# Kernel tuning notes

Hardware: AMD Instinct MI355X
Metric: run time of the kernel (lower is better)

Reference implementation:

```python
import jax, jax.numpy as jnp
import numpy as np

C = 512
CQ = C // 8
BN_EPS = 1e-5


def setup_inputs() -> dict:
    key = jax.random.key(0)
    ks = jax.random.split(key, 12)
    s = 0.02
    return {
        "x": jax.random.normal(ks[0], (4, C, 64, 64), dtype=jnp.float32),
        "qw": jax.random.normal(ks[1], (CQ, C), dtype=jnp.float32) * s,
        "qb": jnp.zeros((CQ,), dtype=jnp.float32),
        "kw": jax.random.normal(ks[2], (CQ, C), dtype=jnp.float32) * s,
        "kb": jnp.zeros((CQ,), dtype=jnp.float32),
        "vw": jax.random.normal(ks[3], (C, C), dtype=jnp.float32) * s,
        "vb": jnp.zeros((C,), dtype=jnp.float32),
        "gamma": jnp.zeros((1,), dtype=jnp.float32),
        "beta": jnp.zeros((1,), dtype=jnp.float32),
        "fw": jax.random.normal(ks[4], (C, 2 * C), dtype=jnp.float32) * s,
        "fb": jnp.zeros((C,), dtype=jnp.float32),
        "bn_w": jnp.ones((C,), dtype=jnp.float32),
        "bn_b": jnp.zeros((C,), dtype=jnp.float32),
    }


def reference(x, qw, qb, kw, kb, vw, vb, gamma, beta, fw, fb, bn_w, bn_b):
    b, c, h, w = x.shape
    n = h * w
    xf = x.reshape(b, c, n)  # [b, c, n]

    # ----- position attention -----
    q = jnp.einsum('oc,bcn->bon', qw, xf) + qb[None, :, None]  # [b, cq, n]
    k = jnp.einsum('oc,bcn->bon', kw, xf) + kb[None, :, None]
    v = jnp.einsum('oc,bcn->bon', vw, xf) + vb[None, :, None]  # [b, c, n]
    # scores[i, j] = q_i . k_j, softmax over j
    scores = jnp.einsum('bci,bcj->bij', q, k)  # [b, n, n]
    att = jax.nn.softmax(scores, axis=-1)
    pos = jnp.einsum('bcj,bij->bci', v, att)  # [b, c, n]
    pos_out = (gamma[0] * pos + xf).reshape(b, c, h, w)

    # ----- channel attention -----
    energy = jnp.einsum('bin,bjn->bij', xf, xf)  # [b, c, c]
    catt = jax.nn.softmax(energy, axis=-1)
    chan = jnp.einsum('bij,bjn->bin', catt, xf)
    chan_out = (beta[0] * chan + xf).reshape(b, c, h, w)

    # ----- fusion: 1x1 conv + BN (batch stats, training mode) + ReLU -----
    cat = jnp.concatenate([pos_out, chan_out], axis=1)  # [b, 2c, h, w]
    y = jnp.einsum('oc,bchw->bohw', fw, cat) + fb[None, :, None, None]
    mean = jnp.mean(y, axis=(0, 2, 3), keepdims=True)
    var = jnp.var(y, axis=(0, 2, 3), keepdims=True)
    yn = (y - mean) * jax.lax.rsqrt(var + BN_EPS)
    out = jax.nn.relu(yn * bn_w[None, :, None, None] + bn_b[None, :, None, None])
    return out
```

## Files before the change

kernel.cpp:

```cpp
#include <hip/hip_runtime.h>
#include <stdint.h>

typedef unsigned short u16;
typedef __attribute__((ext_vector_type(8))) short bf16x8;
typedef __attribute__((ext_vector_type(4))) float f32x4;

#define DEVI static __device__ __forceinline__

DEVI u16 f2bf(float f){
  union { float f; uint32_t u; } c; c.f = f;
  uint32_t u = c.u;
  u += 0x7FFFu + ((u >> 16) & 1u);
  return (u16)(u >> 16);
}
DEVI float b2f(u16 h){
  union { uint32_t u; float f; } c; c.u = ((uint32_t)h) << 16;
  return c.f;
}

DEVI void gload16(const u16* g, u16* l){
  __builtin_amdgcn_global_load_lds(
      (const __attribute__((address_space(1))) unsigned int*)g,
      (__attribute__((address_space(3))) unsigned int*)l, 16, 0, 0);
}

DEVI bf16x8 ldsrd(const void* base, int byte){
  return *reinterpret_cast<const bf16x8*>((const char*)base + byte);
}

template<int BM,int BN,int FM,int FN,int BIAS,int EPI,int SWZ,int KSPLIT=1>
__global__ __launch_bounds__(256) void gemm_bt(
    const u16* __restrict__ A, long long strideA, int lda,
    const u16* __restrict__ B, long long strideB, int ldb,
    void* __restrict__ C, long long strideC, int ldc,
    const float* __restrict__ bias, int K,
    const float* __restrict__ cscale, const u16* __restrict__ xadd,
    long long strideX, int ldx, float* __restrict__ red)
{
  constexpr int BK  = 32;
  constexpr int WTM = FM*16, WTN = FN*16;
  static_assert(BM == 2*WTM && BN == 2*WTN, "2x2 wave layout");
  __shared__ u16 As[BM*BK];
  __shared__ u16 Bs[BN*BK];

  int bx = blockIdx.x, by = blockIdx.y, bz = blockIdx.z;
  if(SWZ){
    const int gx = gridDim.x, gy = gridDim.y;
    const int nwg = gx * gy * gridDim.z;
    const int orig = bx + gx * (by + gy * bz);
    const int q = nwg >> 3, r = nwg & 7;
    const int xcd = orig & 7, i = orig >> 3;
    const int wg = (xcd < r ? xcd*(q+1) : r*(q+1) + (xcd-r)*q) + i;
    bx = wg % gx;
    const int t = wg / gx;
    by = t % gy;
    bz = t / gy;
  }

  const int zz = bz;
  const int z  = (KSPLIT > 1) ? zz / KSPLIT : zz;
  const int ks = (KSPLIT > 1) ? zz % KSPLIT : 0;
  const u16* Ab = A + (long long)z * strideA + (long long)ks * K;
  const u16* Bb = B + (long long)z * strideB + (long long)ks * K;

  const int tid  = threadIdx.x;
  const int lane = tid & 63, wid = tid >> 6;
  const int wr = wid >> 1, wc = wid & 1;
  const long long bm0 = (long long)by * BM;
  const long long bn0 = (long long)bx * BN;

  const int srow  = lane >> 2;
  const int scol  = (((lane & 3) ^ ((lane >> 3) & 3))) * 8;
  const int wrow  = wid * 16 + srow;
  constexpr int TA = BM/64, TB = BN/64;

  const int fr  = lane & 15;
  const int sl8 = ((lane >> 4) ^ ((lane >> 1) & 3)) * 8;

  f32x4 acc[FM][FN] = {};

  for(int k0 = 0; k0 < K; k0 += BK){
    __syncthreads();
    #pragma unroll
    for(int t=0;t<TA;t++)
      gload16(&Ab[(bm0 + t*64 + wrow)*lda + k0 + scol],
              &As[(t*64 + wid*16)*BK]);
    #pragma unroll
    for(int t=0;t<TB;t++)
      gload16(&Bb[(bn0 + t*64 + wrow)*ldb + k0 + scol],
              &Bs[(t*64 + wid*16)*BK]);
    __syncthreads();

    bf16x8 af[FM], bg[FN];
    #pragma unroll
    for(int m=0;m<FM;m++)
      af[m] = *reinterpret_cast<const bf16x8*>(&As[(wr*WTM + m*16 + fr)*BK + sl8]);
    #pragma unroll
    for(int n=0;n<FN;n++)
      bg[n] = *reinterpret_cast<const bf16x8*>(&Bs[(wc*WTN + n*16 + fr)*BK + sl8]);
    #pragma unroll
    for(int m=0;m<FM;m++)
      #pragma unroll
      for(int n=0;n<FN;n++)
        acc[m][n] = __builtin_amdgcn_mfma_f32_16x16x32_bf16(af[m], bg[n], acc[m][n], 0, 0, 0);
  }

  const int lr = (lane >> 4) * 4, lc = lane & 15;

  if(EPI == 7){
    u16* Cp = (u16*)C + (long long)zz*strideC;
    #pragma unroll
    for(int m=0;m<FM;m++){
      #pragma unroll
      for(int r=0;r<4;r++){
        long long row = bm0 + wr*WTM + m*16 + lr + r;
        float bv = bias[(int)row];
        float s = 0.f, ss = 0.f;
        #pragma unroll
        for(int n=0;n<FN;n++){
          long long col = bn0 + wc*WTN + n*16 + lc;
          float v = acc[m][n][r] + bv;
          Cp[row*(long long)ldc + col] = f2bf(v);
          s += v; ss += v*v;
        }
        #pragma unroll
        for(int o=1;o<16;o<<=1){ s += __shfl_xor(s, o); ss += __shfl_xor(ss, o); }
        if(lc == 0){
          int slot = (z*(int)gridDim.x + bx)*2 + wc;
          red[(int)row*512 + slot*2]     = s;
          red[(int)row*512 + slot*2 + 1] = ss;
        }
      }
    }
    return;
  }

  const float g = (EPI == 3) ? cscale[0] : 0.f;
  #pragma unroll
  for(int m=0;m<FM;m++){
    #pragma unroll
    for(int n=0;n<FN;n++){
      #pragma unroll
      for(int r=0;r<4;r++){
        long long row = bm0 + wr*WTM + m*16 + lr + r;
        long long col = bn0 + wc*WTN + n*16 + lc;
        float v = acc[m][n][r];
        if(BIAS == 1) v += bias[(int)row];
        if(BIAS == 2) v += bias[(int)col];
        long long idx = row * (long long)ldc + col;
        if(EPI == 0){
          ((float*)C + (long long)zz*strideC)[idx] = v;
        } else if(EPI == 1){
          ((float*)C + (long long)zz*strideC)[idx] += v;
        } else if(EPI == 2){
          ((u16*)C + (long long)zz*strideC)[idx] = f2bf(v);
        } else {
          float xv = b2f(xadd[(long long)z*strideX + row*(long long)ldx + col]);
          ((u16*)C + (long long)zz*strideC)[idx] = f2bf(g * v + xv);
        }
      }
    }
  }
}

__global__ __launch_bounds__(512, 4) void flash_pos(
    const u16* __restrict__ qkT,
    const u16* __restrict__ vB,
    const u16* __restrict__ xfT,
    u16* __restrict__ pcT,
    const float* __restrict__ gamma)
{
  __shared__ u16 Ks[2][64*64];
  __shared__ u16 Vs[256*64];
  __shared__ u16 Ps[64*64];
  __shared__ float RS[2][4][32];

  int flat = blockIdx.x + 64*(blockIdx.y + 2*blockIdx.z);
  flat = (flat & 7)*64 + (flat >> 3);
  const int bx = flat & 63;
  const int ch = (flat >> 6) & 1;
  const int z  = flat >> 7;

  const int q0 = bx*64, c0 = ch*256;
  const int tid = threadIdx.x, lane = tid & 63, wid = tid >> 6;
  const int wr = wid >> 2, wc = wid & 3;
  const int fr = lane & 15, fq = lane >> 4;

  const u16* qkb = qkT + (long long)z*4096*128;
  const u16* vbb = vB  + (long long)z*512*4096;

  const int srow  = lane >> 3;
  const int sslot = (lane & 7) ^ srow;

  bf16x8 qa[2][2];
  #pragma unroll
  for(int m=0;m<2;m++)
    #pragma unroll
    for(int kk=0;kk<2;kk++)
      qa[m][kk] = *reinterpret_cast<const bf16x8*>(
          &qkb[(long long)(q0 + wr*32 + m*16 + fr)*128 + kk*32 + fq*8]);

  const u16* kp  = qkb + (long long)(wid*8 + srow)*128 + 64 + sslot*8;
  const u16* vp0 = vbb + (long long)(c0 + wid*8 + srow)*4096 + sslot*8;

  const int xm   = (fr & 7) << 4;
  const int koff = (wc*16 + fr)*128 + ((fq*16) ^ xm);
  const int pab  = (wr*32 + fr)*128 + ((fq*16) ^ xm);
  const int vfb  = (wc*64 + fr)*128 + ((fq*16) ^ xm);
  const int kdst = wid * 1024;
  const int key2 = (wc*16 + fr)*2;
  int pwo[4];
  #pragma unroll
  for(int r=0;r<4;r++){
    int qr = fq*4 + r;
    pwo[r] = qr*128 + (key2 ^ ((qr & 7) << 4));
  }

  gload16(kp, (u16*)((char*)Ks + kdst));
  kp += 64*128;
  gload16(vp0,            &Vs[(  0 + wid*8)*64]);
  gload16(vp0 +  64*4096, &Vs[( 64 + wid*8)*64]);
  gload16(vp0 + 128*4096, &Vs[(128 + wid*8)*64]);
  gload16(vp0 + 192*4096, &Vs[(192 + wid*8)*64]);
  vp0 += 64;
  __syncthreads();

  f32x4 acc[2][4] = {};
  float rsacc[2][4] = {};

  for(int t=0;t<64;t++){
    const int kbase = (t & 1) ? 8192 : 0;
    bf16x8 kb0 = ldsrd(Ks, kbase + koff);
    bf16x8 kb1 = ldsrd(Ks, kbase + (koff ^ 64));
    f32x4 s[2] = {};
    #pragma unroll
    for(int m=0;m<2;m++){
      s[m] = __builtin_amdgcn_mfma_f32_16x16x32_bf16(qa[m][0], kb0, s[m], 0, 0, 0);
      s[m] = __builtin_amdgcn_mfma_f32_16x16x32_bf16(qa[m][1], kb1, s[m], 0, 0, 0);
    }

    #pragma unroll
    for(int m=0;m<2;m++){
      #pragma unroll
      for(int r=0;r<4;r++){
        float e = __expf(s[m][r]);
        rsacc[m][r] += e;
        *(u16*)((char*)Ps + (pwo[r] + wr*4096 + m*2048)) = f2bf(e);
      }
    }
    __syncthreads();

    if(t+1 < 64){
      gload16(kp, (u16*)((char*)Ks + (kbase ^ 8192) + kdst));
      kp += 64*128;
    }

    bf16x8 pa00 = ldsrd(Ps, pab);
    bf16x8 pa01 = ldsrd(Ps, pab ^ 64);
    bf16x8 pa10 = ldsrd(Ps, (pab + 2048));
    bf16x8 pa11 = ldsrd(Ps, (pab + 2048) ^ 64);
    __builtin_amdgcn_s_setprio(1);
    #pragma unroll
    for(int n=0;n<4;n++){
      bf16x8 v0 = ldsrd(Vs, vfb + n*2048);
      bf16x8 v1 = ldsrd(Vs, (vfb + n*2048) ^ 64);
      acc[0][n] = __builtin_amdgcn_mfma_f32_16x16x32_bf16(pa00, v0, acc[0][n], 0, 0, 0);
      acc[0][n] = __builtin_amdgcn_mfma_f32_16x16x32_bf16(pa01, v1, acc[0][n], 0, 0, 0);
      acc[1][n] = __builtin_amdgcn_mfma_f32_16x16x32_bf16(pa10, v0, acc[1][n], 0, 0, 0);
      acc[1][n] = __builtin_amdgcn_mfma_f32_16x16x32_bf16(pa11, v1, acc[1][n], 0, 0, 0);
    }
    __builtin_amdgcn_s_setprio(0);
    __syncthreads();

    if(t+1 < 64){
      gload16(vp0,            &Vs[(  0 + wid*8)*64]);
      gload16(vp0 +  64*4096, &Vs[( 64 + wid*8)*64]);
      gload16(vp0 + 128*4096, &Vs[(128 + wid*8)*64]);
      gload16(vp0 + 192*4096, &Vs[(192 + wid*8)*64]);
      vp0 += 64;
    }
  }

  #pragma unroll
  for(int m=0;m<2;m++)
    #pragma unroll
    for(int r=0;r<4;r++){
      float v = rsacc[m][r];
      #pragma unroll
      for(int o=1;o<16;o<<=1) v += __shfl_xor(v, o);
      rsacc[m][r] = v;
    }
  if(fr == 0){
    #pragma unroll
    for(int m=0;m<2;m++)
      #pragma unroll
      for(int r=0;r<4;r++)
        RS[wr][wc][m*16 + fq*4 + r] = rsacc[m][r];
  }
  __syncthreads();

  const float g = gamma[0];
  #pragma unroll
  for(int m=0;m<2;m++){
    float inv[4];
    #pragma unroll
    for(int r=0;r<4;r++){
      int rloc = m*16 + fq*4 + r;
      inv[r] = g / (RS[wr][0][rloc] + RS[wr][1][rloc] +
                    RS[wr][2][rloc] + RS[wr][3][rloc]);
    }
    #pragma unroll
    for(int n=0;n<4;n++){
      #pragma unroll
      for(int r=0;r<4;r++){
        int qrow = q0 + wr*32 + m*16 + fq*4 + r;
        int c    = c0 + wc*64 + n*16 + fr;
        float xv = b2f(xfT[((long long)z*4096 + qrow)*512 + c]);
        pcT[((long long)z*4096 + qrow)*1024 + c] = f2bf(acc[m][n][r]*inv[r] + xv);
      }
    }
  }
}

__global__ __launch_bounds__(256) void softmax_sum8b(const u16* __restrict__ part,
                                                     u16* __restrict__ catt)
{
  const int row = blockIdx.x;
  const int b = row >> 9, i = row & 511;
  const int t = threadIdx.x;
  const int lane = t & 63, wid = t >> 6;
  float v0 = 0.f, v1 = 0.f;
  #pragma unroll
  for(int sl=0;sl<8;sl++){
    uint32_t pr = *reinterpret_cast<const uint32_t*>(
        &part[(((long long)(b*8 + sl)*512 + i)*512) + 2*t]);
    v0 += b2f((u16)pr);
    v1 += b2f((u16)(pr >> 16));
  }
  float m = fmaxf(v0, v1);
  #pragma unroll
  for(int o=32;o;o>>=1) m = fmaxf(m, __shfl_xor(m, o));
  __shared__ float sred[4];
  if(lane == 0) sred[wid] = m;
  __syncthreads();
  m = fmaxf(fmaxf(sred[0], sred[1]), fmaxf(sred[2], sred[3]));
  float e0 = __expf(v0 - m), e1 = __expf(v1 - m);
  float s = e0 + e1;
  #pragma unroll
  for(int o=32;o;o>>=1) s += __shfl_xor(s, o);
  __syncthreads();
  if(lane == 0) sred[wid] = s;
  __syncthreads();
  s = sred[0] + sred[1] + sred[2] + sred[3];
  float inv = 1.0f / s;
  uint32_t pk = (uint32_t)f2bf(e0 * inv) | ((uint32_t)f2bf(e1 * inv) << 16);
  *reinterpret_cast<uint32_t*>(&catt[(long long)row * 512 + 2*t]) = pk;
}

__global__ __launch_bounds__(256) void prep_weights(
    const float* __restrict__ qw, const float* __restrict__ kw,
    const float* __restrict__ vw, const float* __restrict__ fw,
    const float* __restrict__ qb, const float* __restrict__ kb,
    u16* __restrict__ qkwb, u16* __restrict__ vwb, u16* __restrict__ fwb,
    float* __restrict__ qkb)
{
  long long i = (long long)blockIdx.x*256 + threadIdx.x;
  const float* src; u16* dst; long long o;
  if(i < 8192){        src = qw; dst = qkwb;          o = i; }
  else if(i < 16384){  src = kw; dst = qkwb + 32768;  o = i - 8192; }
  else if(i < 81920){  src = vw; dst = vwb;           o = i - 16384; }
  else if(i < 212992){ src = fw; dst = fwb;           o = i - 81920; }
  else if(i < 213024){
    int t = (int)(i - 212992) * 4;
    #pragma unroll
    for(int j=0;j<4;j++) qkb[t+j] = (t+j < 64) ? qb[t+j] : kb[t+j-64];
    return;
  } else return;
  float4 v = reinterpret_cast<const float4*>(src)[o];
  ushort4 w;
  w.x = f2bf(v.x); w.y = f2bf(v.y); w.z = f2bf(v.z); w.w = f2bf(v.w);
  reinterpret_cast<ushort4*>(dst)[o] = w;
}

__global__ __launch_bounds__(256) void transpose_cast(
    const float* __restrict__ x, u16* __restrict__ xfb, u16* __restrict__ xfT)
{
  __shared__ float tile[32][33];
  const int b  = blockIdx.z;
  const int n0 = blockIdx.x * 32, c0 = blockIdx.y * 32;
  const int tx = threadIdx.x, ty = threadIdx.y;
  const float* xp = x + (long long)b * 512 * 4096;
  #pragma unroll
  for(int i=0;i<4;i++){
    int c = c0 + ty + i*8;
    float v = xp[(long long)c*4096 + n0 + tx];
    tile[ty + i*8][tx] = v;
    xfb[((long long)b*512 + c)*4096 + n0 + tx] = f2bf(v);
  }
  __syncthreads();
  #pragma unroll
  for(int i=0;i<4;i++){
    int n = n0 + ty + i*8;
    xfT[((long long)b*4096 + n)*512 + c0 + tx] = f2bf(tile[tx][ty + i*8]);
  }
}

__global__ __launch_bounds__(256) void bn_finalize(const float* __restrict__ red,
                                                   float* __restrict__ stat)
{
  int ch = blockIdx.x*256 + threadIdx.x;
  if(ch >= 512) return;
  float s = 0.f, ss = 0.f;
  for(int j=0;j<256;j++){
    s  += red[ch*512 + j*2];
    ss += red[ch*512 + j*2 + 1];
  }
  float mean = s * (1.f/16384.f);
  float var  = ss * (1.f/16384.f) - mean*mean;
  stat[ch*2]   = mean;
  stat[ch*2+1] = rsqrtf(var + 1e-5f);
}

__global__ __launch_bounds__(256) void bn_apply_b(const u16* __restrict__ y,
    const float* __restrict__ stat, const float* __restrict__ w,
    const float* __restrict__ bb, float* __restrict__ out)
{
  long long i = (long long)blockIdx.x*256 + threadIdx.x;
  bf16x8 v = *reinterpret_cast<const bf16x8*>(&y[i*8]);
  int o = (int)(((i*8) >> 12) & 511);
  float sc = w[o] * stat[o*2+1];
  float sh = bb[o] - stat[o*2] * sc;
  float4 lo, hi;
  lo.x = fmaxf(b2f((u16)v[0])*sc + sh, 0.f);
  lo.y = fmaxf(b2f((u16)v[1])*sc + sh, 0.f);
  lo.z = fmaxf(b2f((u16)v[2])*sc + sh, 0.f);
  lo.w = fmaxf(b2f((u16)v[3])*sc + sh, 0.f);
  hi.x = fmaxf(b2f((u16)v[4])*sc + sh, 0.f);
  hi.y = fmaxf(b2f((u16)v[5])*sc + sh, 0.f);
  hi.z = fmaxf(b2f((u16)v[6])*sc + sh, 0.f);
  hi.w = fmaxf(b2f((u16)v[7])*sc + sh, 0.f);
  *reinterpret_cast<float4*>(&out[i*8])     = lo;
  *reinterpret_cast<float4*>(&out[i*8 + 4]) = hi;
}

extern "C" void kernel_launch(void* const* d_in, const int* in_sizes, int n_in,
                              void* d_out, int out_size, void* d_ws, size_t ws_size,
                              hipStream_t stream)
{
  const float* x     = (const float*)d_in[0];
  const float* qw    = (const float*)d_in[1];
  const float* qb    = (const float*)d_in[2];
  const float* kw    = (const float*)d_in[3];
  const float* kb    = (const float*)d_in[4];
  const float* vw    = (const float*)d_in[5];
  const float* vb    = (const float*)d_in[6];
  const float* gamma = (const float*)d_in[7];
  const float* beta  = (const float*)d_in[8];
  const float* fw    = (const float*)d_in[9];
  const float* fb    = (const float*)d_in[10];
  const float* bnw   = (const float*)d_in[11];
  const float* bnb   = (const float*)d_in[12];
  float* out = (float*)d_out;
  (void)in_sizes; (void)n_in; (void)out_size; (void)ws_size;

  char* base = (char*)d_ws;
  size_t off = 0;
  auto alloc = [&](size_t bytes)->char* {
    char* p = base + off;
    off += (bytes + 255) & ~(size_t)255;
    return p;
  };
  const long long NB = 4, Cc = 512, Nn = 4096;

  u16*   xfT  = (u16*)alloc((size_t)NB*Nn*Cc*2);
  u16*   fwb  = (u16*)alloc((size_t)Cc*2*Cc*2);
  char*  region = (char*)(base + off);
  u16*   xfb  = (u16*)alloc((size_t)NB*Cc*Nn*2);
  u16*   qkwb = (u16*)alloc((size_t)128*Cc*2);
  float* qkb  = (float*)alloc(128*4);
  u16*   vwb  = (u16*)alloc((size_t)Cc*Cc*2);
  u16*   qkT  = (u16*)alloc((size_t)NB*Nn*128*2);
  u16*   vB   = (u16*)alloc((size_t)NB*Cc*Nn*2);
  u16*   pcT  = (u16*)alloc((size_t)NB*Nn*1024*2);
  u16*   epart= (u16*)alloc((size_t)32*Cc*Cc*2);
  u16*   catt = (u16*)alloc((size_t)NB*Cc*Cc*2);
  float* stat = (float*)alloc((size_t)Cc*2*4);
  float* red  = (float*)alloc((size_t)Cc*256*2*4);
  u16*   ybf16= (u16*)region;

  prep_weights<<<dim3(833), dim3(256), 0, stream>>>(qw, kw, vw, fw, qb, kb,
                                                    qkwb, vwb, fwb, qkb);
  transpose_cast<<<dim3(128,16,4), dim3(32,8), 0, stream>>>(x, xfb, xfT);

  gemm_bt<64,128,2,4,2,2,1><<<dim3(1,64,4), dim3(256), 0, stream>>>(
      xfT, Nn*Cc, 512, qkwb, 0, 512, qkT, Nn*128, 128, qkb, 512,
      nullptr, nullptr, 0, 0, nullptr);
  gemm_bt<128,128,4,4,1,2,1><<<dim3(32,4,4), dim3(256), 0, stream>>>(
      vwb, 0, 512, xfT, Nn*Cc, 512, vB, Cc*Nn, 4096, vb, 512,
      nullptr, nullptr, 0, 0, nullptr);

  gemm_bt<128,128,4,4,0,2,1,8><<<dim3(4,4,32), dim3(256), 0, stream>>>(
      xfb, Cc*Nn, 4096, xfb, Cc*Nn, 4096, epart, Cc*Cc, 512, nullptr, 512,
      nullptr, nullptr, 0, 0, nullptr);
  softmax_sum8b<<<dim3(2048), dim3(256), 0, stream>>>(epart, catt);
  gemm_bt<128,128,4,4,0,3,1><<<dim3(4,32,4), dim3(256), 0, stream>>>(
      xfT, Nn*Cc, 512, catt, Cc*Cc, 512, pcT + 512, Nn*1024, 1024, nullptr, 512,
      beta, xfT, Nn*Cc, 512, nullptr);

  flash_pos<<<dim3(64,2,4), dim3(512), 0, stream>>>(qkT, vB, xfT, pcT, gamma);

  gemm_bt<128,128,4,4,1,7,1><<<dim3(32,4,4), dim3(256), 0, stream>>>(
      fwb, 0, 1024, pcT, Nn*1024, 1024, ybf16, Cc*Nn, 4096, fb, 1024,
      nullptr, nullptr, 0, 0, red);

  bn_finalize<<<dim3(2), dim3(256), 0, stream>>>(red, stat);
  bn_apply_b<<<dim3(4096), dim3(256), 0, stream>>>(ybf16, stat, bnw, bnb, out);
}
```

Baseline: 252.7 us.

## Compute fusion GEMM transposed, reduce BN stats per column, transpose in apply

The final 1x1-conv GEMM now has the spatial dimension as rows and output channels as columns, writing a transposed bf16 intermediate with column bias. BN partial sums are reduced down rows per column using fewer shuffles. bn_finalize is parallelized to one block per channel with a wave-shuffle reduction, and bn_apply becomes an LDS-tiled transpose back to NCHW. This trades a cheaper GEMM epilogue and finalize for a less efficient strided, transposing apply kernel.

```diff
diff --git a/kernel.cpp b/kernel.cpp
--- a/kernel.cpp
+++ b/kernel.cpp
@@ -107,29 +107,29 @@
 
   const int lr = (lane >> 4) * 4, lc = lane & 15;
 
-  if(EPI == 7){
+  if(EPI == 9){
     u16* Cp = (u16*)C + (long long)zz*strideC;
     #pragma unroll
-    for(int m=0;m<FM;m++){
-      #pragma unroll
-      for(int r=0;r<4;r++){
-        long long row = bm0 + wr*WTM + m*16 + lr + r;
-        float bv = bias[(int)row];
-        float s = 0.f, ss = 0.f;
+    for(int n=0;n<FN;n++){
+      long long col = bn0 + wc*WTN + n*16 + lc;
+      float bv = bias[(int)col];
+      float s = 0.f, ss = 0.f;
+      #pragma unroll
+      for(int m=0;m<FM;m++){
         #pragma unroll
-        for(int n=0;n<FN;n++){
-          long long col = bn0 + wc*WTN + n*16 + lc;
+        for(int r=0;r<4;r++){
+          long long row = bm0 + wr*WTM + m*16 + lr + r;
           float v = acc[m][n][r] + bv;
           Cp[row*(long long)ldc + col] = f2bf(v);
           s += v; ss += v*v;
         }
-        #pragma unroll
-        for(int o=1;o<16;o<<=1){ s += __shfl_xor(s, o); ss += __shfl_xor(ss, o); }
-        if(lc == 0){
-          int slot = (z*(int)gridDim.x + bx)*2 + wc;
-          red[(int)row*512 + slot*2]     = s;
-          red[(int)row*512 + slot*2 + 1] = ss;
-        }
+      }
+      s += __shfl_xor(s,16); ss += __shfl_xor(ss,16);
+      s += __shfl_xor(s,32); ss += __shfl_xor(ss,32);
+      if(lane < 16){
+        int slot = (z*(int)gridDim.y + by)*2 + wr;
+        red[col*512 + slot*2]     = s;
+        red[col*512 + slot*2 + 1] = ss;
       }
     }
     return;
@@ -408,39 +408,48 @@
 __global__ __launch_bounds__(256) void bn_finalize(const float* __restrict__ red,
                                                    float* __restrict__ stat)
 {
-  int ch = blockIdx.x*256 + threadIdx.x;
-  if(ch >= 512) return;
-  float s = 0.f, ss = 0.f;
-  for(int j=0;j<256;j++){
-    s  += red[ch*512 + j*2];
-    ss += red[ch*512 + j*2 + 1];
-  }
-  float mean = s * (1.f/16384.f);
-  float var  = ss * (1.f/16384.f) - mean*mean;
-  stat[ch*2]   = mean;
-  stat[ch*2+1] = rsqrtf(var + 1e-5f);
-}
-
-__global__ __launch_bounds__(256) void bn_apply_b(const u16* __restrict__ y,
+  const int ch = blockIdx.x;
+  const int t = threadIdx.x, lane = t & 63, wid = t >> 6;
+  float2 p = reinterpret_cast<const float2*>(red)[ch*256 + t];
+  float s = p.x, ss = p.y;
+  #pragma unroll
+  for(int o=32;o;o>>=1){ s += __shfl_xor(s,o); ss += __shfl_xor(ss,o); }
+  __shared__ float sr[8];
+  if(lane == 0){ sr[wid] = s; sr[wid+4] = ss; }
+  __syncthreads();
+  if(t == 0){
+    float S  = sr[0]+sr[1]+sr[2]+sr[3];
+    float SS = sr[4]+sr[5]+sr[6]+sr[7];
+    float mean = S * (1.f/16384.f);
+    float var  = SS * (1.f/16384.f) - mean*mean;
+    stat[ch*2]   = mean;
+    stat[ch*2+1] = rsqrtf(var + 1e-5f);
+  }
+}
+
+__global__ __launch_bounds__(256) void bn_apply_t(const u16* __restrict__ yT,
     const float* __restrict__ stat, const float* __restrict__ w,
     const float* __restrict__ bb, float* __restrict__ out)
 {
-  long long i = (long long)blockIdx.x*256 + threadIdx.x;
-  bf16x8 v = *reinterpret_cast<const bf16x8*>(&y[i*8]);
-  int o = (int)(((i*8) >> 12) & 511);
-  float sc = w[o] * stat[o*2+1];
-  float sh = bb[o] - stat[o*2] * sc;
-  float4 lo, hi;
-  lo.x = fmaxf(b2f((u16)v[0])*sc + sh, 0.f);
-  lo.y = fmaxf(b2f((u16)v[1])*sc + sh, 0.f);
-  lo.z = fmaxf(b2f((u16)v[2])*sc + sh, 0.f);
-  lo.w = fmaxf(b2f((u16)v[3])*sc + sh, 0.f);
-  hi.x = fmaxf(b2f((u16)v[4])*sc + sh, 0.f);
-  hi.y = fmaxf(b2f((u16)v[5])*sc + sh, 0.f);
-  hi.z = fmaxf(b2f((u16)v[6])*sc + sh, 0.f);
-  hi.w = fmaxf(b2f((u16)v[7])*sc + sh, 0.f);
-  *reinterpret_cast<float4*>(&out[i*8])     = lo;
-  *reinterpret_cast<float4*>(&out[i*8 + 4]) = hi;
+  __shared__ float tile[32][33];
+  const int b  = blockIdx.z;
+  const int n0 = blockIdx.x * 32, c0 = blockIdx.y * 32;
+  const int tx = threadIdx.x, ty = threadIdx.y;
+  const int ch = c0 + tx;
+  const float sc = w[ch] * stat[ch*2+1];
+  const float sh = bb[ch] - stat[ch*2] * sc;
+  #pragma unroll
+  for(int i=0;i<4;i++){
+    int n = n0 + ty + i*8;
+    float v = b2f(yT[((long long)b*4096 + n)*512 + ch]);
+    tile[ty + i*8][tx] = fmaxf(v*sc + sh, 0.f);
+  }
+  __syncthreads();
+  #pragma unroll
+  for(int i=0;i<4;i++){
+    int c = c0 + ty + i*8;
+    out[((long long)b*512 + c)*4096 + n0 + tx] = tile[tx][ty + i*8];
+  }
 }
 
 extern "C" void kernel_launch(void* const* d_in, const int* in_sizes, int n_in,
@@ -486,7 +495,7 @@
   u16*   catt = (u16*)alloc((size_t)NB*Cc*Cc*2);
   float* stat = (float*)alloc((size_t)Cc*2*4);
   float* red  = (float*)alloc((size_t)Cc*256*2*4);
-  u16*   ybf16= (u16*)region;
+  u16*   yT   = (u16*)region;
 
   prep_weights<<<dim3(833), dim3(256), 0, stream>>>(qw, kw, vw, fw, qb, kb,
                                                     qkwb, vwb, fwb, qkb);
@@ -509,10 +518,10 @@
 
   flash_pos<<<dim3(64,2,4), dim3(512), 0, stream>>>(qkT, vB, xfT, pcT, gamma);
 
-  gemm_bt<128,128,4,4,1,7,1><<<dim3(32,4,4), dim3(256), 0, stream>>>(
-      fwb, 0, 1024, pcT, Nn*1024, 1024, ybf16, Cc*Nn, 4096, fb, 1024,
+  gemm_bt<128,128,4,4,2,9,1><<<dim3(4,32,4), dim3(256), 0, stream>>>(
+      pcT, Nn*1024, 1024, fwb, 0, 1024, yT, Nn*Cc, 512, fb, 1024,
       nullptr, nullptr, 0, 0, red);
 
-  bn_finalize<<<dim3(2), dim3(256), 0, stream>>>(red, stat);
-  bn_apply_b<<<dim3(4096), dim3(256), 0, stream>>>(ybf16, stat, bnw, bnb, out);
-}
+  bn_finalize<<<dim3(512), dim3(256), 0, stream>>>(red, stat);
+  bn_apply_t<<<dim3(128,16,4), dim3(32,8), 0, stream>>>(yT, stat, bnw, bnb, out);
+}
```

Measured after the change: 234.4 us (median of 2 runs). -7.2%, faster.
